# Optimization experiments

Measured on AMD Instinct MI355X. Metric: run time of the kernel, lower is better.

## Reference

```python
import jax, jax.numpy as jnp
import numpy as np

B, Q, C, P, A = 32, 300, 81, 300, 29


def box_cxcywh_to_xyxy(b):
    cx, cy, w, h = b[..., 0], b[..., 1], b[..., 2], b[..., 3]
    return jnp.stack([cx - 0.5 * w, cy - 0.5 * h, cx + 0.5 * w, cy + 0.5 * h], axis=-1)


def setup_inputs() -> dict:
    key = jax.random.key(0)
    k1, k2, k3, k4, k5 = jax.random.split(key, 5)
    pred_logits = jax.random.normal(k1, (B, Q, C), dtype=jnp.float32)
    pred_boxes = jax.random.uniform(k2, (B, Q, 4), dtype=jnp.float32)
    pred_actions = jax.random.normal(k3, (B, P, A), dtype=jnp.float32)
    pred_rel_pairs = jax.random.randint(k4, (B, P, 2), 0, Q, dtype=jnp.int64)
    # realistic image sizes (h, w) in pixels
    target_sizes = 480.0 + 320.0 * jax.random.uniform(k5, (B, 2), dtype=jnp.float32)
    return {
        'pred_logits': pred_logits,
        'pred_boxes': pred_boxes,
        'pred_actions': pred_actions,
        'pred_rel_pairs': pred_rel_pairs,
        'target_sizes': target_sizes,
    }


def reference(pred_logits, pred_boxes, pred_actions, pred_rel_pairs, target_sizes):
    threshold = 0.0
    # class scores/labels (last class is no-object, excluded from max)
    prob = jax.nn.softmax(pred_logits, axis=-1)
    scores = prob[..., :-1].max(-1)          # [B,Q]
    labels = prob[..., :-1].argmax(-1)       # [B,Q]
    # boxes to xyxy, scaled to image size
    boxes = box_cxcywh_to_xyxy(pred_boxes)   # [B,Q,4]
    img_h, img_w = target_sizes[:, 0], target_sizes[:, 1]
    scale_fct = jnp.stack([img_w, img_h, img_w, img_h], axis=1)  # [B,4]
    boxes = boxes * scale_fct[:, None, :]
    # vcoco path: pairwise action score matrix via one fused scatter
    pair_actions = jax.nn.sigmoid(pred_actions)          # [B,P,A]
    h_idx = pred_rel_pairs[:, :, 0]                      # [B,P]
    o_idx = pred_rel_pairs[:, :, 1]                      # [B,P]
    # original: if h_idx == o_idx -> o_idx = -1 (i.e. last column K of K+1)
    o_idx = jnp.where(h_idx == o_idx, Q, o_idx)
    b_idx = jnp.arange(B, dtype=h_idx.dtype)[:, None]    # [B,1] -> broadcast [B,P]
    score = jnp.zeros((B, Q, Q + 1, A), dtype=pair_actions.dtype)
    score = score.at[b_idx, h_idx, o_idx].set(pair_actions)
    score = jnp.transpose(score, (0, 3, 1, 2))           # [B,A,Q,Q+1]
    # ragged boolean masks (returned as masks instead of data-dependent slices)
    h_mask = (labels == 1) & (scores > threshold)        # human rows
    o_mask = jnp.concatenate([scores > threshold,
                              jnp.ones((B, 1), dtype=bool)], axis=1)  # K+1 cols
    return scores, labels, boxes, score, h_mask, o_mask
```

## Files before the change

### kernel.cpp

```cpp
#include <hip/hip_runtime.h>
#include <hip/hip_bf16.h>

#define BB 32
#define QQ 300
#define CC 81
#define PP 300
#define AA 29

constexpr long long OFF_SCORES = 0;
constexpr long long OFF_LABELS = OFF_SCORES + (long long)BB * QQ;
constexpr long long OFF_BOXES  = OFF_LABELS + (long long)BB * QQ;
constexpr long long OFF_SCORE  = OFF_BOXES  + (long long)BB * QQ * 4;
constexpr long long SCORE_ELEMS = (long long)BB * AA * QQ * (QQ + 1);
constexpr long long OFF_HMASK  = OFF_SCORE + SCORE_ELEMS;
constexpr long long OFF_OMASK  = OFF_HMASK + (long long)BB * QQ;

constexpr int SLOTS = QQ * (QQ + 1);
constexpr int SLOT4 = SLOTS / 4;
constexpr size_t LUT_BYTES = (size_t)BB * SLOTS * sizeof(int);

typedef float f32x4 __attribute__((ext_vector_type(4)));

__global__ __launch_bounds__(512) void lut_build_kernel(const int* __restrict__ pairs,
                                                        int* __restrict__ lut) {
    __shared__ int nz;
    int tid = threadIdx.x;
    int b = blockIdx.x;
    if (tid == 0) nz = 0;
    __syncthreads();

    int local = 0;
    for (int i = tid; i < BB * PP; i += blockDim.x) local |= pairs[2 * i + 1];
    if (local) atomicOr(&nz, 1);

    int4* lb4 = (int4*)(lut + b * SLOTS);
    int4 m1 = make_int4(-1, -1, -1, -1);
    for (int i = tid; i < SLOT4; i += blockDim.x) lb4[i] = m1;
    __syncthreads();
    bool is64 = (nz == 0);

    if (tid < PP) {
        int h, o;
        if (is64) {
            h = pairs[((long long)(b * PP + tid)) * 4 + 0];
            o = pairs[((long long)(b * PP + tid)) * 4 + 2];
        } else {
            h = pairs[((long long)(b * PP + tid)) * 2 + 0];
            o = pairs[((long long)(b * PP + tid)) * 2 + 1];
        }
        if (h == o) o = QQ;
        atomicMax(&lut[b * SLOTS + h * (QQ + 1) + o], tid);
    }
}

__global__ void cls_box_mask_kernel(const float* __restrict__ logits,
                                    const float* __restrict__ boxes_in,
                                    const float* __restrict__ tsize,
                                    float* __restrict__ out) {
    int t = blockIdx.x * blockDim.x + threadIdx.x;
    if (t >= BB * QQ) return;
    int b = t / QQ;
    int q = t - b * QQ;

    const float* l = logits + (long long)t * CC;

    float m = -1e30f;
    float best = -1e30f;
    int am = 0;
    for (int c = 0; c < CC; ++c) {
        float x = l[c];
        m = fmaxf(m, x);
        if (c < CC - 1 && x > best) { best = x; am = c; }
    }
    float s = 0.0f;
    for (int c = 0; c < CC; ++c) {
        s += __expf(l[c] - m);
    }
    float score = __expf(best - m) / s;

    out[OFF_SCORES + t] = score;
    out[OFF_LABELS + t] = (float)am;

    float cx = boxes_in[4 * (long long)t + 0];
    float cy = boxes_in[4 * (long long)t + 1];
    float w  = boxes_in[4 * (long long)t + 2];
    float h  = boxes_in[4 * (long long)t + 3];
    float img_h = tsize[2 * b + 0];
    float img_w = tsize[2 * b + 1];
    out[OFF_BOXES + 4 * (long long)t + 0] = (cx - 0.5f * w) * img_w;
    out[OFF_BOXES + 4 * (long long)t + 1] = (cy - 0.5f * h) * img_h;
    out[OFF_BOXES + 4 * (long long)t + 2] = (cx + 0.5f * w) * img_w;
    out[OFF_BOXES + 4 * (long long)t + 3] = (cy + 0.5f * h) * img_h;

    out[OFF_HMASK + t] = (am == 1 && score > 0.0f) ? 1.0f : 0.0f;
    out[OFF_OMASK + (long long)b * (QQ + 1) + q] = (score > 0.0f) ? 1.0f : 0.0f;
    if (q == 0) out[OFF_OMASK + (long long)b * (QQ + 1) + QQ] = 1.0f;
}

__global__ __launch_bounds__(256) void score_write_kernel(const int* __restrict__ lut,
                                                          const float* __restrict__ actions,
                                                          float* __restrict__ out) {
    int a = blockIdx.x;
    int chunk = blockIdx.y;
    int b = blockIdx.z;
    const int4* lb4 = (const int4*)(lut + b * SLOTS);
    const float* actb = actions + (long long)b * PP * AA + a;
    f32x4* plane4 = (f32x4*)(out + OFF_SCORE + (long long)(b * AA + a) * SLOTS);

    int s4 = chunk * 1024 + threadIdx.x;
    #pragma unroll
    for (int k = 0; k < 4; ++k, s4 += 256) {
        if (s4 >= SLOT4) break;
        int4 pi = lb4[s4];
        f32x4 v = (f32x4)0.0f;
        if (pi.x >= 0) v.x = 1.0f / (1.0f + __expf(-actb[pi.x * AA]));
        if (pi.y >= 0) v.y = 1.0f / (1.0f + __expf(-actb[pi.y * AA]));
        if (pi.z >= 0) v.z = 1.0f / (1.0f + __expf(-actb[pi.z * AA]));
        if (pi.w >= 0) v.w = 1.0f / (1.0f + __expf(-actb[pi.w * AA]));
        plane4[s4] = v;
    }
}

__global__ void scatter_kernel(const int* __restrict__ pairs,
                               const float* __restrict__ actions,
                               float* __restrict__ out) {
    __shared__ int keys[PP];
    __shared__ int nz;
    int tid = threadIdx.x;
    if (tid == 0) nz = 0;
    __syncthreads();

    int local = 0;
    for (int i = tid; i < BB * PP; i += blockDim.x) local |= pairs[2 * i + 1];
    if (local) atomicOr(&nz, 1);
    __syncthreads();
    bool is64 = (nz == 0);

    int b = blockIdx.x;
    int p = tid;
    int h = -1, o = -1;
    if (p < PP) {
        if (is64) {
            h = pairs[((long long)(b * PP + p)) * 4 + 0];
            o = pairs[((long long)(b * PP + p)) * 4 + 2];
        } else {
            h = pairs[((long long)(b * PP + p)) * 2 + 0];
            o = pairs[((long long)(b * PP + p)) * 2 + 1];
        }
        if (h == o) o = QQ;
        keys[p] = h * (QQ + 1) + o;
    }
    __syncthreads();
    if (p >= PP) return;

    int k = keys[p];
    for (int p2 = p + 1; p2 < PP; ++p2) {
        if (keys[p2] == k) return;
    }

    const float* act = actions + (long long)(b * PP + p) * AA;
    long long base = OFF_SCORE + (long long)b * AA * QQ * (QQ + 1)
                   + (long long)h * (QQ + 1) + o;
    for (int a = 0; a < AA; ++a) {
        float x = act[a];
        float sg = 1.0f / (1.0f + __expf(-x));
        out[base + (long long)a * QQ * (QQ + 1)] = sg;
    }
}

extern "C" void kernel_launch(void* const* d_in, const int* in_sizes, int n_in,
                              void* d_out, int out_size, void* d_ws, size_t ws_size,
                              hipStream_t stream) {
    const float* logits   = (const float*)d_in[0];
    const float* boxes_in = (const float*)d_in[1];
    const float* actions  = (const float*)d_in[2];
    const int*   pairs    = (const int*)d_in[3];
    const float* tsize    = (const float*)d_in[4];
    float* out = (float*)d_out;

    int n = BB * QQ;
    if (d_ws != nullptr && ws_size >= LUT_BYTES) {
        int* lut = (int*)d_ws;
        lut_build_kernel<<<BB, 512, 0, stream>>>(pairs, lut);
        cls_box_mask_kernel<<<(n + 255) / 256, 256, 0, stream>>>(logits, boxes_in, tsize, out);
        score_write_kernel<<<dim3(AA, (SLOT4 + 1023) / 1024, BB), 256, 0, stream>>>(lut, actions, out);
    } else {
        hipMemsetAsync((char*)d_out + OFF_SCORE * sizeof(float), 0,
                       (size_t)SCORE_ELEMS * sizeof(float), stream);
        cls_box_mask_kernel<<<(n + 255) / 256, 256, 0, stream>>>(logits, boxes_in, tsize, out);
        scatter_kernel<<<BB, 320, 0, stream>>>(pairs, actions, out);
    }
}
```

Before: 414.1 us.

## Reuse LUT across all actions per block and split LUT init into grid-wide kernel

The score kernel now loads each LUT chunk once and loops over all 29 action planes, writing one plane after another, instead of launching a block per action that re-reads the LUT. It also skips sigmoid work for int4 groups with no hits. LUT initialisation moves into its own grid-wide fill kernel, so the 32 scatter blocks no longer do the large memset. In exchange the score grid shrinks from 29*23*32 blocks to 23*32 = 736 blocks, each doing far more writes, which may reduce parallelism and memory-level concurrency. It also adds one more kernel launch.

New measurement: 431.6 us. +4.2%, slower.

```diff
diff --git a/kernel.cpp b/kernel.cpp
--- a/kernel.cpp
+++ b/kernel.cpp
@@ -17,25 +17,30 @@
 
 constexpr int SLOTS = QQ * (QQ + 1);
 constexpr int SLOT4 = SLOTS / 4;
+constexpr int CHUNKS = (SLOT4 + 1023) / 1024;
 constexpr size_t LUT_BYTES = (size_t)BB * SLOTS * sizeof(int);
 
 typedef float f32x4 __attribute__((ext_vector_type(4)));
 
-__global__ __launch_bounds__(512) void lut_build_kernel(const int* __restrict__ pairs,
-                                                        int* __restrict__ lut) {
+__global__ __launch_bounds__(256) void lut_init_kernel(int* __restrict__ lut) {
+    int4* p = (int4*)lut;
+    const int n4 = BB * SLOTS / 4;
+    int i = blockIdx.x * blockDim.x + threadIdx.x;
+    const int stride = gridDim.x * blockDim.x;
+    int4 m1 = make_int4(-1, -1, -1, -1);
+    for (; i < n4; i += stride) p[i] = m1;
+}
+
+__global__ __launch_bounds__(320) void lut_scatter_kernel(const int* __restrict__ pairs,
+                                                          int* __restrict__ lut) {
     __shared__ int nz;
     int tid = threadIdx.x;
     int b = blockIdx.x;
     if (tid == 0) nz = 0;
     __syncthreads();
-
     int local = 0;
     for (int i = tid; i < BB * PP; i += blockDim.x) local |= pairs[2 * i + 1];
     if (local) atomicOr(&nz, 1);
-
-    int4* lb4 = (int4*)(lut + b * SLOTS);
-    int4 m1 = make_int4(-1, -1, -1, -1);
-    for (int i = tid; i < SLOT4; i += blockDim.x) lb4[i] = m1;
     __syncthreads();
     bool is64 = (nz == 0);
 
@@ -100,24 +105,40 @@
 __global__ __launch_bounds__(256) void score_write_kernel(const int* __restrict__ lut,
                                                           const float* __restrict__ actions,
                                                           float* __restrict__ out) {
-    int a = blockIdx.x;
-    int chunk = blockIdx.y;
-    int b = blockIdx.z;
+    int chunk = blockIdx.x;
+    int b = blockIdx.y;
     const int4* lb4 = (const int4*)(lut + b * SLOTS);
-    const float* actb = actions + (long long)b * PP * AA + a;
-    f32x4* plane4 = (f32x4*)(out + OFF_SCORE + (long long)(b * AA + a) * SLOTS);
-
-    int s4 = chunk * 1024 + threadIdx.x;
+    const float* actb = actions + (long long)b * PP * AA;
+    float* plane0 = out + OFF_SCORE + (long long)b * AA * SLOTS;
+
+    int q0 = chunk * 1024 + threadIdx.x;
+
+    int4 pi[4];
+    bool valid[4];
+    bool anyhit[4];
     #pragma unroll
-    for (int k = 0; k < 4; ++k, s4 += 256) {
-        if (s4 >= SLOT4) break;
-        int4 pi = lb4[s4];
-        f32x4 v = (f32x4)0.0f;
-        if (pi.x >= 0) v.x = 1.0f / (1.0f + __expf(-actb[pi.x * AA]));
-        if (pi.y >= 0) v.y = 1.0f / (1.0f + __expf(-actb[pi.y * AA]));
-        if (pi.z >= 0) v.z = 1.0f / (1.0f + __expf(-actb[pi.z * AA]));
-        if (pi.w >= 0) v.w = 1.0f / (1.0f + __expf(-actb[pi.w * AA]));
-        plane4[s4] = v;
+    for (int k = 0; k < 4; ++k) {
+        int q = q0 + k * 256;
+        valid[k] = (q < SLOT4);
+        pi[k] = valid[k] ? lb4[q] : make_int4(-1, -1, -1, -1);
+        int mx = max(max(pi[k].x, pi[k].y), max(pi[k].z, pi[k].w));
+        anyhit[k] = (mx >= 0);
+    }
+
+    for (int a = 0; a < AA; ++a) {
+        f32x4* pl = (f32x4*)(plane0 + (long long)a * SLOTS);
+        #pragma unroll
+        for (int k = 0; k < 4; ++k) {
+            if (!valid[k]) continue;
+            f32x4 v = (f32x4)0.0f;
+            if (anyhit[k]) {
+                if (pi[k].x >= 0) v.x = 1.0f / (1.0f + __expf(-actb[pi[k].x * AA + a]));
+                if (pi[k].y >= 0) v.y = 1.0f / (1.0f + __expf(-actb[pi[k].y * AA + a]));
+                if (pi[k].z >= 0) v.z = 1.0f / (1.0f + __expf(-actb[pi[k].z * AA + a]));
+                if (pi[k].w >= 0) v.w = 1.0f / (1.0f + __expf(-actb[pi[k].w * AA + a]));
+            }
+            pl[q0 + k * 256] = v;
+        }
     }
 }
 
@@ -181,9 +202,10 @@
     int n = BB * QQ;
     if (d_ws != nullptr && ws_size >= LUT_BYTES) {
         int* lut = (int*)d_ws;
-        lut_build_kernel<<<BB, 512, 0, stream>>>(pairs, lut);
+        lut_init_kernel<<<1024, 256, 0, stream>>>(lut);
+        lut_scatter_kernel<<<BB, 320, 0, stream>>>(pairs, lut);
         cls_box_mask_kernel<<<(n + 255) / 256, 256, 0, stream>>>(logits, boxes_in, tsize, out);
-        score_write_kernel<<<dim3(AA, (SLOT4 + 1023) / 1024, BB), 256, 0, stream>>>(lut, actions, out);
+        score_write_kernel<<<dim3(CHUNKS, BB), 256, 0, stream>>>(lut, actions, out);
     } else {
         hipMemsetAsync((char*)d_out + OFF_SCORE * sizeof(float), 0,
                        (size_t)SCORE_ELEMS * sizeof(float), stream);
```
